# Kernel tuning notes

Hardware: AMD Instinct MI355X
Metric: run time of the kernel (lower is better)

## Reference

```python
import jax, jax.numpy as jnp
import numpy as np

B, S, D, H = 4, 2048, 512, 8
DH = D // H  # 64


def setup_inputs() -> dict:
    key = jax.random.key(0)
    ks = jax.random.split(key, 7)
    scale = 1.0 / np.sqrt(D)
    return {
        "in_query": jax.random.normal(ks[0], (B, S, D), dtype=jnp.float32),
        "in_key": jax.random.normal(ks[1], (B, S, D), dtype=jnp.float32),
        "in_value": jax.random.normal(ks[2], (B, S, D), dtype=jnp.float32),
        "W_q": jax.random.normal(ks[3], (D, D), dtype=jnp.float32) * scale,
        "W_k": jax.random.normal(ks[4], (D, D), dtype=jnp.float32) * scale,
        "W_v": jax.random.normal(ks[5], (D, D), dtype=jnp.float32) * scale,
        "W_out": jax.random.normal(ks[6], (D, D), dtype=jnp.float32) * scale,
    }


def _split_heads(x):
    # [B, S, D] -> [B, H, S, DH]
    return x.reshape(B, S, H, DH).transpose(0, 2, 1, 3)


def reference(in_query, in_key, in_value, W_q, W_k, W_v, W_out):
    q = _split_heads(in_query @ W_q)   # [B,H,S,DH]
    k = _split_heads(in_key @ W_k)
    v = _split_heads(in_value @ W_v)
    scores = jnp.einsum("bhqd,bhkd->bhqk", q, k) / jnp.sqrt(jnp.float32(DH))
    attn = jax.nn.softmax(scores, axis=-1)  # dropout p=0 -> identity
    out = jnp.einsum("bhqk,bhkd->bhqd", attn, v)  # [B,H,S,DH]
    out = out.transpose(0, 2, 1, 3).reshape(B, S, D)
    return out @ W_out
```

## Files before the change

kernel.cpp:

```cpp
#include <hip/hip_runtime.h>
#include <hip/hip_bf16.h>
#include <cstdint>
#include <cstddef>


typedef __bf16 bf16;
typedef __attribute__((ext_vector_type(8))) __bf16 bf16x8;
typedef __attribute__((ext_vector_type(4))) __bf16 bf16x4;
typedef __attribute__((ext_vector_type(4))) float floatx4;

#define MFMA16(a, b, c) __builtin_amdgcn_mfma_f32_16x16x32_bf16(a, b, c, 0, 0, 0)

#define GLD16(gp, lp)                                              \
  __builtin_amdgcn_global_load_lds(                                \
      (const __attribute__((address_space(1))) unsigned int*)(gp), \
      (__attribute__((address_space(3))) unsigned int*)(lp), 16, 0, 0)

#define PIPE_TOP()                                     \
  do {                                                 \
    asm volatile("s_waitcnt vmcnt(0)" ::: "memory");   \
    __builtin_amdgcn_s_barrier();                      \
    __builtin_amdgcn_sched_barrier(0);                 \
  } while (0)

__device__ __forceinline__ void split2(float x, bf16& hi, bf16& lo) {
  hi = (bf16)x;
  lo = (bf16)(x - (float)hi);
}

__global__ __launch_bounds__(256) void k_split_w(
    const float* __restrict__ Wq, const float* __restrict__ Wk,
    const float* __restrict__ Wv, const float* __restrict__ Wo,
    bf16* __restrict__ wt_hi, bf16* __restrict__ wt_lo) {
  __shared__ float tile[64][65];
  const int w = blockIdx.z;
  const float* W = (w == 0) ? Wq : (w == 1) ? Wk : (w == 2) ? Wv : Wo;
  const int kb = blockIdx.y * 64, nb = blockIdx.x * 64;
  const int tid = threadIdx.x;
  const int col = tid & 63, rbase = tid >> 6;
#pragma unroll
  for (int i = 0; i < 16; i++) {
    int row = rbase + i * 4;
    tile[row][col] = W[(size_t)(kb + row) * 512 + nb + col];
  }
  __syncthreads();
#pragma unroll
  for (int i = 0; i < 16; i++) {
    int nrow = rbase + i * 4;
    float v = tile[col][nrow];
    bf16 hi, lo;
    split2(v, hi, lo);
    size_t o = (size_t)w * 262144 + (size_t)(nb + nrow) * 512 + (kb + col);
    wt_hi[o] = hi;
    wt_lo[o] = lo;
  }
}

__global__ __launch_bounds__(256, 2) void k_proj_qkv(
    const float* __restrict__ Xq, const float* __restrict__ Xk,
    const float* __restrict__ Xv,
    const bf16* __restrict__ wt_hi, const bf16* __restrict__ wt_lo,
    bf16* __restrict__ Q_hi, bf16* __restrict__ Q_lo,
    bf16* __restrict__ K, bf16* __restrict__ Vt) {
  const int P = blockIdx.x;
  const int c_all = P >> 5, within = P & 31;
  const int n_idx = within >> 3, i8 = within & 7;
  const int which = c_all >> 3;
  const int g = ((c_all & 7) << 3) | i8;
  const int m0 = g * 128, n0 = n_idx * 128;

  const float* X = (which == 0) ? Xq : (which == 1) ? Xk : Xv;
  const uint8_t* Bhb = (const uint8_t*)(wt_hi + (size_t)which * 262144);
  const uint8_t* Blb = (const uint8_t*)(wt_lo + (size_t)which * 262144);
  const uint8_t* Xb = (const uint8_t*)X;
  const int tid = threadIdx.x, wave = tid >> 6, lane = tid & 63;
  const int l15 = lane & 15, l4 = lane >> 4;
  const int Am0 = (wave & 1) * 64, Bn0 = (wave >> 1) * 64;

  __shared__ float sA[2][128 * 32];
  __shared__ bf16 sBh[2][128 * 32], sBl[2][128 * 32];

  int aoff[4], adst[4];
#pragma unroll
  for (int p = 0; p < 4; p++) {
    int slot = p * 256 + tid;
    int row = slot >> 3, phys = slot & 7, lg = phys ^ (row & 7);
    aoff[p] = (m0 + row) * 2048 + lg * 16;
    adst[p] = slot * 16;
  }
  int boff[2], bdst[2];
#pragma unroll
  for (int p = 0; p < 2; p++) {
    int slot = p * 256 + tid;
    int row = slot >> 2, phys = slot & 3, lg = phys ^ (row & 3);
    boff[p] = (n0 + row) * 1024 + lg * 16;
    bdst[p] = slot * 16;
  }

  floatx4 acc[4][4];
#pragma unroll
  for (int i = 0; i < 4; i++)
#pragma unroll
    for (int j = 0; j < 4; j++) acc[i][j] = {0.f, 0.f, 0.f, 0.f};

#pragma unroll
  for (int p = 0; p < 4; p++) GLD16(Xb + aoff[p], (char*)sA[0] + adst[p]);
#pragma unroll
  for (int p = 0; p < 2; p++) {
    GLD16(Bhb + boff[p], (char*)sBh[0] + bdst[p]);
    GLD16(Blb + boff[p], (char*)sBl[0] + bdst[p]);
  }

  int cur = 0;
  for (int kb = 0; kb < 512; kb += 32) {
    PIPE_TOP();

    const char* cA = (const char*)sA[cur];
    const char* cBh = (const char*)sBh[cur];
    const char* cBl = (const char*)sBl[cur];

    floatx4 af0[4], af1[4];
    bf16x8 bhf[4], blf[4];
#pragma unroll
    for (int mt = 0; mt < 4; mt++) {
      int row = Am0 + mt * 16 + l15, r7 = row & 7;
      af0[mt] = *(const floatx4*)(cA + row * 128 + (((2 * l4) ^ r7) * 16));
      af1[mt] = *(const floatx4*)(cA + row * 128 + (((2 * l4 + 1) ^ r7) * 16));
    }
#pragma unroll
    for (int nt = 0; nt < 4; nt++) {
      int row = Bn0 + nt * 16 + l15, r3 = row & 3;
      bhf[nt] = *(const bf16x8*)(cBh + row * 64 + ((l4 ^ r3) * 16));
      blf[nt] = *(const bf16x8*)(cBl + row * 64 + ((l4 ^ r3) * 16));
    }

    if (kb + 32 < 512) {
      const int nx = cur ^ 1, nkb = kb + 32;
#pragma unroll
      for (int p = 0; p < 4; p++)
        GLD16(Xb + aoff[p] + nkb * 4, (char*)sA[nx] + adst[p]);
#pragma unroll
      for (int p = 0; p < 2; p++) {
        GLD16(Bhb + boff[p] + nkb * 2, (char*)sBh[nx] + bdst[p]);
        GLD16(Blb + boff[p] + nkb * 2, (char*)sBl[nx] + bdst[p]);
      }
    }

    bf16x8 ah[4], al[4];
#pragma unroll
    for (int mt = 0; mt < 4; mt++) {
#pragma unroll
      for (int j = 0; j < 4; j++) {
        bf16 h, l;
        split2(af0[mt][j], h, l);
        ah[mt][j] = h; al[mt][j] = l;
        split2(af1[mt][j], h, l);
        ah[mt][4 + j] = h; al[mt][4 + j] = l;
      }
    }
#pragma unroll
    for (int nt = 0; nt < 4; nt++) {
#pragma unroll
      for (int mt = 0; mt < 4; mt++) {
        acc[mt][nt] = MFMA16(ah[mt], bhf[nt], acc[mt][nt]);
        acc[mt][nt] = MFMA16(ah[mt], blf[nt], acc[mt][nt]);
        acc[mt][nt] = MFMA16(al[mt], bhf[nt], acc[mt][nt]);
      }
    }
    cur ^= 1;
  }

  const float scale = (which == 0) ? 0.125f : (which == 1) ? 1.44269504f : 1.0f;
#pragma unroll
  for (int mt = 0; mt < 4; mt++) {
#pragma unroll
    for (int nt = 0; nt < 4; nt++) {
      int m_base = m0 + Am0 + mt * 16 + l4 * 4;
      int n = n0 + Bn0 + nt * 16 + l15;
      int h = (n >> 6) & 7, d = n & 63;
      if (which == 2) {
        int kbase = m_base & 2047, b = m_base >> 11;
        int a32 = kbase & ~31, v = (kbase >> 2) & 7;
        int sbase = a32 + 8 * (v & 3) + 4 * (v >> 2);
        bf16x4 pv;
#pragma unroll
        for (int r = 0; r < 4; r++) pv[r] = (bf16)acc[mt][nt][r];
        *(bf16x4*)&Vt[((size_t)(b * 8 + h) * 64 + d) * 2048 + sbase] = pv;
      } else {
#pragma unroll
        for (int r = 0; r < 4; r++) {
          int m = m_base + r;
          int b = m >> 11, s = m & 2047;
          float v = acc[mt][nt][r] * scale;
          size_t o = ((size_t)(b * 8 + h) * 2048 + s) * 64 + d;
          if (which == 0) {
            bf16 hi, lo;
            split2(v, hi, lo);
            Q_hi[o] = hi; Q_lo[o] = lo;
          } else {
            K[o] = (bf16)v;
          }
        }
      }
    }
  }
}

__global__ __launch_bounds__(256, 2) void k_flash(
    const bf16* __restrict__ Q_hi, const bf16* __restrict__ Q_lo,
    const bf16* __restrict__ K, const bf16* __restrict__ Vt,
    bf16* __restrict__ O_hi, bf16* __restrict__ O_lo) {
  const int P = blockIdx.x;
  const int hi4 = P >> 8, rem = P & 255;
  const int qt = rem >> 3;
  const int bh = hi4 * 8 + (rem & 7);
  const int b = bh >> 3, h = bh & 7;
  const int tid = threadIdx.x, wave = tid >> 6, lane = tid & 63;
  const int l15 = lane & 15, l4 = lane >> 4;
  const int q0 = qt * 64;

  __shared__ char smem[2 * 32768 + 1024];
  float* lbuf = (float*)(smem + 65536);

  const uint8_t* Kb = (const uint8_t*)K + (size_t)bh * 2048 * 128;
  const uint8_t* Vb = (const uint8_t*)Vt + (size_t)bh * 64 * 4096;
  int koff[4], voff[4], dst[4];
#pragma unroll
  for (int p = 0; p < 4; p++) {
    int slot = p * 256 + tid;
    {
      int row = slot >> 3, phys = slot & 7, lg = phys ^ (row & 7);
      koff[p] = row * 128 + lg * 16;
    }
    {
      int row = slot >> 4, phys = slot & 15, lg = phys ^ (row & 15);
      voff[p] = row * 4096 + lg * 16;
    }
    dst[p] = slot * 16;
  }

#pragma unroll
  for (int p = 0; p < 4; p++) {
    GLD16(Kb + koff[p], smem + dst[p]);
    GLD16(Vb + voff[p], smem + 16384 + dst[p]);
  }

  bf16x8 qh[4][2], ql[4][2];
#pragma unroll
  for (int nt = 0; nt < 4; nt++) {
    const bf16* ph = Q_hi + ((size_t)bh * 2048 + q0 + nt * 16 + l15) * 64 + l4 * 8;
    const bf16* pl = Q_lo + ((size_t)bh * 2048 + q0 + nt * 16 + l15) * 64 + l4 * 8;
    qh[nt][0] = *(const bf16x8*)ph;
    qh[nt][1] = *(const bf16x8*)(ph + 32);
    ql[nt][0] = *(const bf16x8*)pl;
    ql[nt][1] = *(const bf16x8*)(pl + 32);
  }

  float lp[4] = {0.f, 0.f, 0.f, 0.f};
  floatx4 oacc[4][4];
#pragma unroll
  for (int i = 0; i < 4; i++)
#pragma unroll
    for (int j = 0; j < 4; j++) oacc[i][j] = {0.f, 0.f, 0.f, 0.f};

  int cur = 0;
  for (int j0 = 0; j0 < 2048; j0 += 128) {
    PIPE_TOP();

    const char* sK = smem + cur * 32768;
    const char* sV = sK + 16384;

    bf16x8 kf[2][2];
#pragma unroll
    for (int kt = 0; kt < 2; kt++) {
      int row = wave * 32 + kt * 16 + l15, r7 = row & 7;
#pragma unroll
      for (int ks = 0; ks < 2; ks++)
        kf[ks][kt] =
            *(const bf16x8*)(sK + row * 128 + (((ks * 4 + l4) ^ r7) * 16));
    }
    bf16x8 vf[4];
#pragma unroll
    for (int nt = 0; nt < 4; nt++) {
      int row = nt * 16 + l15;
      vf[nt] =
          *(const bf16x8*)(sV + row * 256 + (((wave * 4 + l4) ^ l15) * 16));
    }

    if (j0 + 128 < 2048) {
      char* nb = smem + (cur ^ 1) * 32768;
      const size_t nj = (size_t)(j0 + 128);
#pragma unroll
      for (int p = 0; p < 4; p++) {
        GLD16(Kb + nj * 128 + koff[p], nb + dst[p]);
        GLD16(Vb + nj * 2 + voff[p], nb + 16384 + dst[p]);
      }
    }

    floatx4 sc[2][4];
#pragma unroll
    for (int kt = 0; kt < 2; kt++)
#pragma unroll
      for (int nt = 0; nt < 4; nt++)
        sc[kt][nt] = {-24.f, -24.f, -24.f, -24.f};
#pragma unroll
    for (int ks = 0; ks < 2; ks++) {
#pragma unroll
      for (int nt = 0; nt < 4; nt++) {
        sc[0][nt] = MFMA16(kf[ks][0], qh[nt][ks], sc[0][nt]);
        sc[0][nt] = MFMA16(kf[ks][0], ql[nt][ks], sc[0][nt]);
        sc[1][nt] = MFMA16(kf[ks][1], qh[nt][ks], sc[1][nt]);
        sc[1][nt] = MFMA16(kf[ks][1], ql[nt][ks], sc[1][nt]);
      }
    }

    bf16x8 pf[4];
#pragma unroll
    for (int nt = 0; nt < 4; nt++) {
#pragma unroll
      for (int r = 0; r < 4; r++) {
        float p0 = __builtin_amdgcn_exp2f(sc[0][nt][r]);
        float p1 = __builtin_amdgcn_exp2f(sc[1][nt][r]);
        lp[nt] += p0 + p1;
        pf[nt][r] = (bf16)p0;
        pf[nt][4 + r] = (bf16)p1;
      }
    }

#pragma unroll
    for (int nt = 0; nt < 4; nt++) {
#pragma unroll
      for (int mq = 0; mq < 4; mq++)
        oacc[mq][nt] = MFMA16(pf[mq], vf[nt], oacc[mq][nt]);
    }
    cur ^= 1;
  }

#pragma unroll
  for (int nt = 0; nt < 4; nt++) {
    lp[nt] += __shfl_xor(lp[nt], 16, 64);
    lp[nt] += __shfl_xor(lp[nt], 32, 64);
  }
  __syncthreads();
  if (l4 == 0) {
#pragma unroll
    for (int nt = 0; nt < 4; nt++) lbuf[wave * 64 + nt * 16 + l15] = lp[nt];
  }
  floatx4* red = (floatx4*)smem;
#pragma unroll
  for (int phase = 0; phase < 2; phase++) {
    if (wave >= 1) {
#pragma unroll
      for (int i = 0; i < 8; i++) {
        int mq = phase * 2 + (i >> 2);
        red[(wave - 1) * 512 + i * 64 + lane] = oacc[mq][i & 3];
      }
    }
    __syncthreads();
    if (wave == 0) {
#pragma unroll
      for (int i = 0; i < 8; i++) {
        int mq = phase * 2 + (i >> 2);
        oacc[mq][i & 3] += red[i * 64 + lane] + red[512 + i * 64 + lane] +
                           red[1024 + i * 64 + lane];
      }
    }
    __syncthreads();
  }
  if (wave == 0) {
    float lt[4];
#pragma unroll
    for (int nt = 0; nt < 4; nt++)
      lt[nt] = lbuf[nt * 16 + l15] + lbuf[64 + nt * 16 + l15] +
               lbuf[128 + nt * 16 + l15] + lbuf[192 + nt * 16 + l15];
    float rl[4][4];
#pragma unroll
    for (int mq = 0; mq < 4; mq++)
#pragma unroll
      for (int r = 0; r < 4; r++)
        rl[mq][r] = 1.0f / __shfl(lt[mq], (lane & 48) | (l4 * 4 + r), 64);
#pragma unroll
    for (int mq = 0; mq < 4; mq++) {
#pragma unroll
      for (int nt = 0; nt < 4; nt++) {
#pragma unroll
        for (int r = 0; r < 4; r++) {
          float v = oacc[mq][nt][r] * rl[mq][r];
          int gs = q0 + mq * 16 + l4 * 4 + r;
          int gd = h * 64 + nt * 16 + l15;
          size_t o = ((size_t)b * 2048 + gs) * 512 + gd;
          bf16 hi, lo;
          split2(v, hi, lo);
          O_hi[o] = hi;
          O_lo[o] = lo;
        }
      }
    }
  }
}

__global__ __launch_bounds__(256, 2) void k_proj_out(
    const bf16* __restrict__ O_hi, const bf16* __restrict__ O_lo,
    const bf16* __restrict__ wt_hi, const bf16* __restrict__ wt_lo,
    float* __restrict__ out) {
  const int P = blockIdx.x;
  const int c = P >> 5, within = P & 31;
  const int n_idx = within >> 3, i8 = within & 7;
  const int g = (c << 3) | i8;
  const int m0 = g * 128, n0 = n_idx * 128;

  const uint8_t* Ahb = (const uint8_t*)O_hi;
  const uint8_t* Alb = (const uint8_t*)O_lo;
  const uint8_t* Bhb = (const uint8_t*)(wt_hi + (size_t)3 * 262144);
  const uint8_t* Blb = (const uint8_t*)(wt_lo + (size_t)3 * 262144);
  const int tid = threadIdx.x, wave = tid >> 6, lane = tid & 63;
  const int l15 = lane & 15, l4 = lane >> 4;
  const int Am0 = (wave & 1) * 64, Bn0 = (wave >> 1) * 64;

  __shared__ bf16 sAh[2][128 * 32], sAl[2][128 * 32];
  __shared__ bf16 sBh[2][128 * 32], sBl[2][128 * 32];

  int aoff[2], boff[2], dst[2];
#pragma unroll
  for (int p = 0; p < 2; p++) {
    int slot = p * 256 + tid;
    int row = slot >> 2, phys = slot & 3, lg = phys ^ (row & 3);
    aoff[p] = (m0 + row) * 1024 + lg * 16;
    boff[p] = (n0 + row) * 1024 + lg * 16;
    dst[p] = slot * 16;
  }

  floatx4 acc[4][4];
#pragma unroll
  for (int i = 0; i < 4; i++)
#pragma unroll
    for (int j = 0; j < 4; j++) acc[i][j] = {0.f, 0.f, 0.f, 0.f};

#pragma unroll
  for (int p = 0; p < 2; p++) {
    GLD16(Ahb + aoff[p], (char*)sAh[0] + dst[p]);
    GLD16(Alb + aoff[p], (char*)sAl[0] + dst[p]);
    GLD16(Bhb + boff[p], (char*)sBh[0] + dst[p]);
    GLD16(Blb + boff[p], (char*)sBl[0] + dst[p]);
  }

  int cur = 0;
  for (int kb = 0; kb < 512; kb += 32) {
    PIPE_TOP();

    const char* cAh = (const char*)sAh[cur];
    const char* cAl = (const char*)sAl[cur];
    const char* cBh = (const char*)sBh[cur];
    const char* cBl = (const char*)sBl[cur];

    bf16x8 ah[4], al[4], bhf[4], blf[4];
#pragma unroll
    for (int mt = 0; mt < 4; mt++) {
      int row = Am0 + mt * 16 + l15, r3 = row & 3;
      ah[mt] = *(const bf16x8*)(cAh + row * 64 + ((l4 ^ r3) * 16));
      al[mt] = *(const bf16x8*)(cAl + row * 64 + ((l4 ^ r3) * 16));
    }
#pragma unroll
    for (int nt = 0; nt < 4; nt++) {
      int row = Bn0 + nt * 16 + l15, r3 = row & 3;
      bhf[nt] = *(const bf16x8*)(cBh + row * 64 + ((l4 ^ r3) * 16));
      blf[nt] = *(const bf16x8*)(cBl + row * 64 + ((l4 ^ r3) * 16));
    }

    if (kb + 32 < 512) {
      const int nx = cur ^ 1, nkb = kb + 32;
#pragma unroll
      for (int p = 0; p < 2; p++) {
        GLD16(Ahb + aoff[p] + nkb * 2, (char*)sAh[nx] + dst[p]);
        GLD16(Alb + aoff[p] + nkb * 2, (char*)sAl[nx] + dst[p]);
        GLD16(Bhb + boff[p] + nkb * 2, (char*)sBh[nx] + dst[p]);
        GLD16(Blb + boff[p] + nkb * 2, (char*)sBl[nx] + dst[p]);
      }
    }

#pragma unroll
    for (int nt = 0; nt < 4; nt++) {
#pragma unroll
      for (int mt = 0; mt < 4; mt++) {
        acc[mt][nt] = MFMA16(ah[mt], bhf[nt], acc[mt][nt]);
        acc[mt][nt] = MFMA16(ah[mt], blf[nt], acc[mt][nt]);
        acc[mt][nt] = MFMA16(al[mt], bhf[nt], acc[mt][nt]);
      }
    }
    cur ^= 1;
  }
#pragma unroll
  for (int mt = 0; mt < 4; mt++) {
#pragma unroll
    for (int nt = 0; nt < 4; nt++) {
#pragma unroll
      for (int r = 0; r < 4; r++) {
        int m = m0 + Am0 + mt * 16 + l4 * 4 + r;
        int n = n0 + Bn0 + nt * 16 + l15;
        out[(size_t)m * 512 + n] = acc[mt][nt][r];
      }
    }
  }
}

extern "C" void kernel_launch(void* const* d_in, const int* in_sizes, int n_in,
                              void* d_out, int out_size, void* d_ws, size_t ws_size,
                              hipStream_t stream) {
  (void)in_sizes; (void)n_in; (void)out_size; (void)ws_size;
  const float* Xq = (const float*)d_in[0];
  const float* Xk = (const float*)d_in[1];
  const float* Xv = (const float*)d_in[2];
  const float* Wq = (const float*)d_in[3];
  const float* Wk = (const float*)d_in[4];
  const float* Wv = (const float*)d_in[5];
  const float* Wo = (const float*)d_in[6];
  float* out = (float*)d_out;

  char* ws = (char*)d_ws;
  size_t off = 0;
  auto alloc = [&](size_t n) {
    void* p = ws + off;
    off += (n + 255) & ~(size_t)255;
    return p;
  };
  const size_t NW = 4 * 262144;
  const size_t NE = 4194304;
  bf16* wt_hi = (bf16*)alloc(NW * 2);
  bf16* wt_lo = (bf16*)alloc(NW * 2);
  bf16* Qh = (bf16*)alloc(NE * 2);
  bf16* Ql = (bf16*)alloc(NE * 2);
  bf16* Kk = (bf16*)alloc(NE * 2);
  bf16* Vt = (bf16*)alloc(NE * 2);
  bf16* Oh = (bf16*)alloc(NE * 2);
  bf16* Ol = (bf16*)alloc(NE * 2);

  k_split_w<<<dim3(8, 8, 4), dim3(256), 0, stream>>>(Wq, Wk, Wv, Wo, wt_hi, wt_lo);
  k_proj_qkv<<<dim3(768), dim3(256), 0, stream>>>(Xq, Xk, Xv, wt_hi, wt_lo,
                                                  Qh, Ql, Kk, Vt);
  k_flash<<<dim3(1024), dim3(256), 0, stream>>>(Qh, Ql, Kk, Vt, Oh, Ol);
  k_proj_out<<<dim3(256), dim3(256), 0, stream>>>(Oh, Ol, wt_hi, wt_lo, out);
}
```

Before: 222.2 us.

## Load A operand and V fragments directly from global into registers

In the QKV projection, the fp32 activation tile is no longer staged through LDS. Each lane loads its A fragments straight from global memory into registers, prefetched one k-step ahead. In the flash kernel, V fragments are read directly from global memory each iteration instead of being double-buffered in LDS. Both changes cut shared-memory use so launch bounds can be raised to 3 blocks per CU for more occupancy. The trade-off is uncoalesced, non-prefetched global loads (especially V in flash, loaded after the barrier with no overlap) and more register pressure under the tighter launch bound.

```diff
diff --git a/kernel.cpp b/kernel.cpp
--- a/kernel.cpp
+++ b/kernel.cpp
@@ -56,7 +56,7 @@
   }
 }
 
-__global__ __launch_bounds__(256, 2) void k_proj_qkv(
+__global__ __launch_bounds__(256, 3) void k_proj_qkv(
     const float* __restrict__ Xq, const float* __restrict__ Xk,
     const float* __restrict__ Xv,
     const bf16* __restrict__ wt_hi, const bf16* __restrict__ wt_lo,
@@ -77,16 +77,13 @@
   const int l15 = lane & 15, l4 = lane >> 4;
   const int Am0 = (wave & 1) * 64, Bn0 = (wave >> 1) * 64;
 
-  __shared__ float sA[2][128 * 32];
   __shared__ bf16 sBh[2][128 * 32], sBl[2][128 * 32];
 
-  int aoff[4], adst[4];
-#pragma unroll
-  for (int p = 0; p < 4; p++) {
-    int slot = p * 256 + tid;
-    int row = slot >> 3, phys = slot & 7, lg = phys ^ (row & 7);
-    aoff[p] = (m0 + row) * 2048 + lg * 16;
-    adst[p] = slot * 16;
+  const uint8_t* aptr[4];
+#pragma unroll
+  for (int mt = 0; mt < 4; mt++) {
+    int row = m0 + Am0 + mt * 16 + l15;
+    aptr[mt] = Xb + (size_t)row * 2048 + l4 * 32;
   }
   int boff[2], bdst[2];
 #pragma unroll
@@ -104,29 +101,26 @@
     for (int j = 0; j < 4; j++) acc[i][j] = {0.f, 0.f, 0.f, 0.f};
 
 #pragma unroll
-  for (int p = 0; p < 4; p++) GLD16(Xb + aoff[p], (char*)sA[0] + adst[p]);
-#pragma unroll
   for (int p = 0; p < 2; p++) {
     GLD16(Bhb + boff[p], (char*)sBh[0] + bdst[p]);
     GLD16(Blb + boff[p], (char*)sBl[0] + bdst[p]);
   }
+  floatx4 af0c[4], af1c[4];
+#pragma unroll
+  for (int mt = 0; mt < 4; mt++) {
+    af0c[mt] = *(const floatx4*)(aptr[mt]);
+    af1c[mt] = *(const floatx4*)(aptr[mt] + 16);
+  }
 
   int cur = 0;
+#pragma unroll 2
   for (int kb = 0; kb < 512; kb += 32) {
     PIPE_TOP();
 
-    const char* cA = (const char*)sA[cur];
     const char* cBh = (const char*)sBh[cur];
     const char* cBl = (const char*)sBl[cur];
 
-    floatx4 af0[4], af1[4];
     bf16x8 bhf[4], blf[4];
-#pragma unroll
-    for (int mt = 0; mt < 4; mt++) {
-      int row = Am0 + mt * 16 + l15, r7 = row & 7;
-      af0[mt] = *(const floatx4*)(cA + row * 128 + (((2 * l4) ^ r7) * 16));
-      af1[mt] = *(const floatx4*)(cA + row * 128 + (((2 * l4 + 1) ^ r7) * 16));
-    }
 #pragma unroll
     for (int nt = 0; nt < 4; nt++) {
       int row = Bn0 + nt * 16 + l15, r3 = row & 3;
@@ -134,16 +128,19 @@
       blf[nt] = *(const bf16x8*)(cBl + row * 64 + ((l4 ^ r3) * 16));
     }
 
+    floatx4 af0n[4], af1n[4];
     if (kb + 32 < 512) {
       const int nx = cur ^ 1, nkb = kb + 32;
-#pragma unroll
-      for (int p = 0; p < 4; p++)
-        GLD16(Xb + aoff[p] + nkb * 4, (char*)sA[nx] + adst[p]);
 #pragma unroll
       for (int p = 0; p < 2; p++) {
         GLD16(Bhb + boff[p] + nkb * 2, (char*)sBh[nx] + bdst[p]);
         GLD16(Blb + boff[p] + nkb * 2, (char*)sBl[nx] + bdst[p]);
       }
+#pragma unroll
+      for (int mt = 0; mt < 4; mt++) {
+        af0n[mt] = *(const floatx4*)(aptr[mt] + nkb * 4);
+        af1n[mt] = *(const floatx4*)(aptr[mt] + nkb * 4 + 16);
+      }
     }
 
     bf16x8 ah[4], al[4];
@@ -152,9 +149,9 @@
 #pragma unroll
       for (int j = 0; j < 4; j++) {
         bf16 h, l;
-        split2(af0[mt][j], h, l);
+        split2(af0c[mt][j], h, l);
         ah[mt][j] = h; al[mt][j] = l;
-        split2(af1[mt][j], h, l);
+        split2(af1c[mt][j], h, l);
         ah[mt][4 + j] = h; al[mt][4 + j] = l;
       }
     }
@@ -166,6 +163,11 @@
         acc[mt][nt] = MFMA16(ah[mt], blf[nt], acc[mt][nt]);
         acc[mt][nt] = MFMA16(al[mt], bhf[nt], acc[mt][nt]);
       }
+    }
+#pragma unroll
+    for (int mt = 0; mt < 4; mt++) {
+      af0c[mt] = af0n[mt];
+      af1c[mt] = af1n[mt];
     }
     cur ^= 1;
   }
@@ -206,7 +208,7 @@
   }
 }
 
-__global__ __launch_bounds__(256, 2) void k_flash(
+__global__ __launch_bounds__(256, 3) void k_flash(
     const bf16* __restrict__ Q_hi, const bf16* __restrict__ Q_lo,
     const bf16* __restrict__ K, const bf16* __restrict__ Vt,
     bf16* __restrict__ O_hi, bf16* __restrict__ O_lo) {
@@ -219,31 +221,22 @@
   const int l15 = lane & 15, l4 = lane >> 4;
   const int q0 = qt * 64;
 
-  __shared__ char smem[2 * 32768 + 1024];
-  float* lbuf = (float*)(smem + 65536);
+  __shared__ char smem[2 * 16384 + 1024];
+  float* lbuf = (float*)(smem + 32768);
 
   const uint8_t* Kb = (const uint8_t*)K + (size_t)bh * 2048 * 128;
   const uint8_t* Vb = (const uint8_t*)Vt + (size_t)bh * 64 * 4096;
-  int koff[4], voff[4], dst[4];
+  int koff[4], dst[4];
 #pragma unroll
   for (int p = 0; p < 4; p++) {
     int slot = p * 256 + tid;
-    {
-      int row = slot >> 3, phys = slot & 7, lg = phys ^ (row & 7);
-      koff[p] = row * 128 + lg * 16;
-    }
-    {
-      int row = slot >> 4, phys = slot & 15, lg = phys ^ (row & 15);
-      voff[p] = row * 4096 + lg * 16;
-    }
+    int row = slot >> 3, phys = slot & 7, lg = phys ^ (row & 7);
+    koff[p] = row * 128 + lg * 16;
     dst[p] = slot * 16;
   }
 
 #pragma unroll
-  for (int p = 0; p < 4; p++) {
-    GLD16(Kb + koff[p], smem + dst[p]);
-    GLD16(Vb + voff[p], smem + 16384 + dst[p]);
-  }
+  for (int p = 0; p < 4; p++) GLD16(Kb + koff[p], smem + dst[p]);
 
   bf16x8 qh[4][2], ql[4][2];
 #pragma unroll
@@ -267,9 +260,15 @@
   for (int j0 = 0; j0 < 2048; j0 += 128) {
     PIPE_TOP();
 
-    const char* sK = smem + cur * 32768;
-    const char* sV = sK + 16384;
-
+    bf16x8 vf[4];
+#pragma unroll
+    for (int nt = 0; nt < 4; nt++) {
+      int row = nt * 16 + l15;
+      vf[nt] = *(const bf16x8*)(Vb + (size_t)row * 4096 + j0 * 2 +
+                                (wave * 4 + l4) * 16);
+    }
+
+    const char* sK = smem + cur * 16384;
     bf16x8 kf[2][2];
 #pragma unroll
     for (int kt = 0; kt < 2; kt++) {
@@ -279,22 +278,12 @@
         kf[ks][kt] =
             *(const bf16x8*)(sK + row * 128 + (((ks * 4 + l4) ^ r7) * 16));
     }
-    bf16x8 vf[4];
-#pragma unroll
-    for (int nt = 0; nt < 4; nt++) {
-      int row = nt * 16 + l15;
-      vf[nt] =
-          *(const bf16x8*)(sV + row * 256 + (((wave * 4 + l4) ^ l15) * 16));
-    }
 
     if (j0 + 128 < 2048) {
-      char* nb = smem + (cur ^ 1) * 32768;
+      char* nb = smem + (cur ^ 1) * 16384;
       const size_t nj = (size_t)(j0 + 128);
 #pragma unroll
-      for (int p = 0; p < 4; p++) {
-        GLD16(Kb + nj * 128 + koff[p], nb + dst[p]);
-        GLD16(Vb + nj * 2 + voff[p], nb + 16384 + dst[p]);
-      }
+      for (int p = 0; p < 4; p++) GLD16(Kb + nj * 128 + koff[p], nb + dst[p]);
     }
 
     floatx4 sc[2][4];
```

New measurement: 403.6 us. +81.6%, slower.

## Single-buffer LDS in all GEMM/flash kernels and raise occupancy to three blocks

Applied to the files above, without the earlier changes.

Replaces double-buffered LDS staging with a single buffer in the QKV projection, flash attention and output projection kernels. A new LDS-wait-plus-barrier is placed before the next prefetch so the buffer can be overwritten safely. Occupancy hints are raised from two to three blocks per CU. Flash now keeps Q hi/lo fragments in LDS instead of registers, and the output projection uses 64-row tiles with twice as many blocks. The aim is more resident waves and better CU fill, at the cost of an extra barrier per iteration and less overlap between loads and compute.

```diff
diff --git a/kernel.cpp b/kernel.cpp
--- a/kernel.cpp
+++ b/kernel.cpp
@@ -19,6 +19,14 @@
 #define PIPE_TOP()                                     \
   do {                                                 \
     asm volatile("s_waitcnt vmcnt(0)" ::: "memory");   \
+    __builtin_amdgcn_s_barrier();                      \
+    __builtin_amdgcn_sched_barrier(0);                 \
+  } while (0)
+
+#define LGKM_BARRIER()                                 \
+  do {                                                 \
+    asm volatile("s_waitcnt lgkmcnt(0)" ::: "memory"); \
+    __builtin_amdgcn_sched_barrier(0);                 \
     __builtin_amdgcn_s_barrier();                      \
     __builtin_amdgcn_sched_barrier(0);                 \
   } while (0)
@@ -56,7 +64,7 @@
   }
 }
 
-__global__ __launch_bounds__(256, 2) void k_proj_qkv(
+__global__ __launch_bounds__(256, 3) void k_proj_qkv(
     const float* __restrict__ Xq, const float* __restrict__ Xk,
     const float* __restrict__ Xv,
     const bf16* __restrict__ wt_hi, const bf16* __restrict__ wt_lo,
@@ -77,8 +85,8 @@
   const int l15 = lane & 15, l4 = lane >> 4;
   const int Am0 = (wave & 1) * 64, Bn0 = (wave >> 1) * 64;
 
-  __shared__ float sA[2][128 * 32];
-  __shared__ bf16 sBh[2][128 * 32], sBl[2][128 * 32];
+  __shared__ float sA[128 * 32];
+  __shared__ bf16 sBh[128 * 32], sBl[128 * 32];
 
   int aoff[4], adst[4];
 #pragma unroll
@@ -104,45 +112,42 @@
     for (int j = 0; j < 4; j++) acc[i][j] = {0.f, 0.f, 0.f, 0.f};
 
 #pragma unroll
-  for (int p = 0; p < 4; p++) GLD16(Xb + aoff[p], (char*)sA[0] + adst[p]);
+  for (int p = 0; p < 4; p++) GLD16(Xb + aoff[p], (char*)sA + adst[p]);
 #pragma unroll
   for (int p = 0; p < 2; p++) {
-    GLD16(Bhb + boff[p], (char*)sBh[0] + bdst[p]);
-    GLD16(Blb + boff[p], (char*)sBl[0] + bdst[p]);
-  }
-
-  int cur = 0;
+    GLD16(Bhb + boff[p], (char*)sBh + bdst[p]);
+    GLD16(Blb + boff[p], (char*)sBl + bdst[p]);
+  }
+
   for (int kb = 0; kb < 512; kb += 32) {
     PIPE_TOP();
 
-    const char* cA = (const char*)sA[cur];
-    const char* cBh = (const char*)sBh[cur];
-    const char* cBl = (const char*)sBl[cur];
-
     floatx4 af0[4], af1[4];
     bf16x8 bhf[4], blf[4];
 #pragma unroll
     for (int mt = 0; mt < 4; mt++) {
       int row = Am0 + mt * 16 + l15, r7 = row & 7;
-      af0[mt] = *(const floatx4*)(cA + row * 128 + (((2 * l4) ^ r7) * 16));
-      af1[mt] = *(const floatx4*)(cA + row * 128 + (((2 * l4 + 1) ^ r7) * 16));
+      af0[mt] = *(const floatx4*)((const char*)sA + row * 128 + (((2 * l4) ^ r7) * 16));
+      af1[mt] = *(const floatx4*)((const char*)sA + row * 128 + (((2 * l4 + 1) ^ r7) * 16));
     }
 #pragma unroll
     for (int nt = 0; nt < 4; nt++) {
       int row = Bn0 + nt * 16 + l15, r3 = row & 3;
-      bhf[nt] = *(const bf16x8*)(cBh + row * 64 + ((l4 ^ r3) * 16));
-      blf[nt] = *(const bf16x8*)(cBl + row * 64 + ((l4 ^ r3) * 16));
-    }
+      bhf[nt] = *(const bf16x8*)((const char*)sBh + row * 64 + ((l4 ^ r3) * 16));
+      blf[nt] = *(const bf16x8*)((const char*)sBl + row * 64 + ((l4 ^ r3) * 16));
+    }
+
+    LGKM_BARRIER();
 
     if (kb + 32 < 512) {
-      const int nx = cur ^ 1, nkb = kb + 32;
+      const int nkb = kb + 32;
 #pragma unroll
       for (int p = 0; p < 4; p++)
-        GLD16(Xb + aoff[p] + nkb * 4, (char*)sA[nx] + adst[p]);
+        GLD16(Xb + aoff[p] + nkb * 4, (char*)sA + adst[p]);
 #pragma unroll
       for (int p = 0; p < 2; p++) {
-        GLD16(Bhb + boff[p] + nkb * 2, (char*)sBh[nx] + bdst[p]);
-        GLD16(Blb + boff[p] + nkb * 2, (char*)sBl[nx] + bdst[p]);
+        GLD16(Bhb + boff[p] + nkb * 2, (char*)sBh + bdst[p]);
+        GLD16(Blb + boff[p] + nkb * 2, (char*)sBl + bdst[p]);
       }
     }
 
@@ -167,7 +172,6 @@
         acc[mt][nt] = MFMA16(al[mt], bhf[nt], acc[mt][nt]);
       }
     }
-    cur ^= 1;
   }
 
   const float scale = (which == 0) ? 0.125f : (which == 1) ? 1.44269504f : 1.0f;
@@ -206,7 +210,7 @@
   }
 }
 
-__global__ __launch_bounds__(256, 2) void k_flash(
+__global__ __launch_bounds__(256, 3) void k_flash(
     const bf16* __restrict__ Q_hi, const bf16* __restrict__ Q_lo,
     const bf16* __restrict__ K, const bf16* __restrict__ Vt,
     bf16* __restrict__ O_hi, bf16* __restrict__ O_lo) {
@@ -219,8 +223,8 @@
   const int l15 = lane & 15, l4 = lane >> 4;
   const int q0 = qt * 64;
 
-  __shared__ char smem[2 * 32768 + 1024];
-  float* lbuf = (float*)(smem + 65536);
+  __shared__ char smem[50176];
+  float* lbuf = (float*)(smem + 49152);
 
   const uint8_t* Kb = (const uint8_t*)K + (size_t)bh * 2048 * 128;
   const uint8_t* Vb = (const uint8_t*)Vt + (size_t)bh * 64 * 4096;
@@ -245,15 +249,19 @@
     GLD16(Vb + voff[p], smem + 16384 + dst[p]);
   }
 
-  bf16x8 qh[4][2], ql[4][2];
 #pragma unroll
   for (int nt = 0; nt < 4; nt++) {
-    const bf16* ph = Q_hi + ((size_t)bh * 2048 + q0 + nt * 16 + l15) * 64 + l4 * 8;
-    const bf16* pl = Q_lo + ((size_t)bh * 2048 + q0 + nt * 16 + l15) * 64 + l4 * 8;
-    qh[nt][0] = *(const bf16x8*)ph;
-    qh[nt][1] = *(const bf16x8*)(ph + 32);
-    ql[nt][0] = *(const bf16x8*)pl;
-    ql[nt][1] = *(const bf16x8*)(pl + 32);
+#pragma unroll
+    for (int ks = 0; ks < 2; ks++) {
+      const bf16* ph =
+          Q_hi + ((size_t)bh * 2048 + q0 + nt * 16 + l15) * 64 + ks * 32 + l4 * 8;
+      const bf16* pl =
+          Q_lo + ((size_t)bh * 2048 + q0 + nt * 16 + l15) * 64 + ks * 32 + l4 * 8;
+      *(bf16x8*)(smem + 32768 + ((nt * 2 + ks) * 64 + lane) * 16) =
+          *(const bf16x8*)ph;
+      *(bf16x8*)(smem + 40960 + ((nt * 2 + ks) * 64 + lane) * 16) =
+          *(const bf16x8*)pl;
+    }
   }
 
   float lp[4] = {0.f, 0.f, 0.f, 0.f};
@@ -263,12 +271,13 @@
 #pragma unroll
     for (int j = 0; j < 4; j++) oacc[i][j] = {0.f, 0.f, 0.f, 0.f};
 
-  int cur = 0;
+  __syncthreads();
+
   for (int j0 = 0; j0 < 2048; j0 += 128) {
     PIPE_TOP();
 
-    const char* sK = smem + cur * 32768;
-    const char* sV = sK + 16384;
+    const char* sK = smem;
+    const char* sV = smem + 16384;
 
     bf16x8 kf[2][2];
 #pragma unroll
@@ -287,13 +296,14 @@
           *(const bf16x8*)(sV + row * 256 + (((wave * 4 + l4) ^ l15) * 16));
     }
 
+    LGKM_BARRIER();
+
     if (j0 + 128 < 2048) {
-      char* nb = smem + (cur ^ 1) * 32768;
       const size_t nj = (size_t)(j0 + 128);
 #pragma unroll
       for (int p = 0; p < 4; p++) {
-        GLD16(Kb + nj * 128 + koff[p], nb + dst[p]);
-        GLD16(Vb + nj * 2 + voff[p], nb + 16384 + dst[p]);
+        GLD16(Kb + nj * 128 + koff[p], smem + dst[p]);
+        GLD16(Vb + nj * 2 + voff[p], smem + 16384 + dst[p]);
       }
     }
 
@@ -307,10 +317,14 @@
     for (int ks = 0; ks < 2; ks++) {
 #pragma unroll
       for (int nt = 0; nt < 4; nt++) {
-        sc[0][nt] = MFMA16(kf[ks][0], qh[nt][ks], sc[0][nt]);
-        sc[0][nt] = MFMA16(kf[ks][0], ql[nt][ks], sc[0][nt]);
-        sc[1][nt] = MFMA16(kf[ks][1], qh[nt][ks], sc[1][nt]);
-        sc[1][nt] = MFMA16(kf[ks][1], ql[nt][ks], sc[1][nt]);
+        bf16x8 qhf =
+            *(const bf16x8*)(smem + 32768 + ((nt * 2 + ks) * 64 + lane) * 16);
+        bf16x8 qlf =
+            *(const bf16x8*)(smem + 40960 + ((nt * 2 + ks) * 64 + lane) * 16);
+        sc[0][nt] = MFMA16(kf[ks][0], qhf, sc[0][nt]);
+        sc[0][nt] = MFMA16(kf[ks][0], qlf, sc[0][nt]);
+        sc[1][nt] = MFMA16(kf[ks][1], qhf, sc[1][nt]);
+        sc[1][nt] = MFMA16(kf[ks][1], qlf, sc[1][nt]);
       }
     }
 
@@ -333,7 +347,6 @@
       for (int mq = 0; mq < 4; mq++)
         oacc[mq][nt] = MFMA16(pf[mq], vf[nt], oacc[mq][nt]);
     }
-    cur ^= 1;
   }
 
 #pragma unroll
@@ -404,10 +417,8 @@
     const bf16* __restrict__ wt_hi, const bf16* __restrict__ wt_lo,
     float* __restrict__ out) {
   const int P = blockIdx.x;
-  const int c = P >> 5, within = P & 31;
-  const int n_idx = within >> 3, i8 = within & 7;
-  const int g = (c << 3) | i8;
-  const int m0 = g * 128, n0 = n_idx * 128;
+  const int g = P & 127, n_idx = P >> 7;
+  const int m0 = g * 64, n0 = n_idx * 128;
 
   const uint8_t* Ahb = (const uint8_t*)O_hi;
   const uint8_t* Alb = (const uint8_t*)O_lo;
@@ -415,82 +426,83 @@
   const uint8_t* Blb = (const uint8_t*)(wt_lo + (size_t)3 * 262144);
   const int tid = threadIdx.x, wave = tid >> 6, lane = tid & 63;
   const int l15 = lane & 15, l4 = lane >> 4;
-  const int Am0 = (wave & 1) * 64, Bn0 = (wave >> 1) * 64;
-
-  __shared__ bf16 sAh[2][128 * 32], sAl[2][128 * 32];
-  __shared__ bf16 sBh[2][128 * 32], sBl[2][128 * 32];
-
-  int aoff[2], boff[2], dst[2];
+  const int Am0 = (wave & 1) * 32, Bn0 = (wave >> 1) * 64;
+
+  __shared__ bf16 sAh[64 * 32], sAl[64 * 32];
+  __shared__ bf16 sBh[128 * 32], sBl[128 * 32];
+
+  int aoff, adst;
+  {
+    int slot = tid;
+    int row = slot >> 2, phys = slot & 3, lg = phys ^ (row & 3);
+    aoff = (m0 + row) * 1024 + lg * 16;
+    adst = slot * 16;
+  }
+  int boff[2], bdst[2];
 #pragma unroll
   for (int p = 0; p < 2; p++) {
     int slot = p * 256 + tid;
     int row = slot >> 2, phys = slot & 3, lg = phys ^ (row & 3);
-    aoff[p] = (m0 + row) * 1024 + lg * 16;
     boff[p] = (n0 + row) * 1024 + lg * 16;
-    dst[p] = slot * 16;
-  }
-
-  floatx4 acc[4][4];
-#pragma unroll
-  for (int i = 0; i < 4; i++)
+    bdst[p] = slot * 16;
+  }
+
+  floatx4 acc[2][4];
+#pragma unroll
+  for (int i = 0; i < 2; i++)
 #pragma unroll
     for (int j = 0; j < 4; j++) acc[i][j] = {0.f, 0.f, 0.f, 0.f};
 
+  GLD16(Ahb + aoff, (char*)sAh + adst);
+  GLD16(Alb + aoff, (char*)sAl + adst);
 #pragma unroll
   for (int p = 0; p < 2; p++) {
-    GLD16(Ahb + aoff[p], (char*)sAh[0] + dst[p]);
-    GLD16(Alb + aoff[p], (char*)sAl[0] + dst[p]);
-    GLD16(Bhb + boff[p], (char*)sBh[0] + dst[p]);
-    GLD16(Blb + boff[p], (char*)sBl[0] + dst[p]);
-  }
-
-  int cur = 0;
+    GLD16(Bhb + boff[p], (char*)sBh + bdst[p]);
+    GLD16(Blb + boff[p], (char*)sBl + bdst[p]);
+  }
+
   for (int kb = 0; kb < 512; kb += 32) {
     PIPE_TOP();
 
-    const char* cAh = (const char*)sAh[cur];
-    const char* cAl = (const char*)sAl[cur];
-    const char* cBh = (const char*)sBh[cur];
-    const char* cBl = (const char*)sBl[cur];
-
-    bf16x8 ah[4], al[4], bhf[4], blf[4];
-#pragma unroll
-    for (int mt = 0; mt < 4; mt++) {
+    bf16x8 ah[2], al[2], bhf[4], blf[4];
+#pragma unroll
+    for (int mt = 0; mt < 2; mt++) {
       int row = Am0 + mt * 16 + l15, r3 = row & 3;
-      ah[mt] = *(const bf16x8*)(cAh + row * 64 + ((l4 ^ r3) * 16));
-      al[mt] = *(const bf16x8*)(cAl + row * 64 + ((l4 ^ r3) * 16));
+      ah[mt] = *(const bf16x8*)((const char*)sAh + row * 64 + ((l4 ^ r3) * 16));
+      al[mt] = *(const bf16x8*)((const char*)sAl + row * 64 + ((l4 ^ r3) * 16));
     }
 #pragma unroll
     for (int nt = 0; nt < 4; nt++) {
       int row = Bn0 + nt * 16 + l15, r3 = row & 3;
-      bhf[nt] = *(const bf16x8*)(cBh + row * 64 + ((l4 ^ r3) * 16));
-      blf[nt] = *(const bf16x8*)(cBl + row * 64 + ((l4 ^ r3) * 16));
-    }
+      bhf[nt] = *(const bf16x8*)((const char*)sBh + row * 64 + ((l4 ^ r3) * 16));
+      blf[nt] = *(const bf16x8*)((const char*)sBl + row * 64 + ((l4 ^ r3) * 16));
+    }
+
+    LGKM_BARRIER();
 
     if (kb + 32 < 512) {
-      const int nx = cur ^ 1, nkb = kb + 32;
+      const int nkb = kb + 32;
+      GLD16(Ahb + aoff + nkb * 2, (char*)sAh + adst);
+      GLD16(Alb + aoff + nkb * 2, (char*)sAl + adst);
 #pragma unroll
       for (int p = 0; p < 2; p++) {
-        GLD16(Ahb + aoff[p] + nkb * 2, (char*)sAh[nx] + dst[p]);
-        GLD16(Alb + aoff[p] + nkb * 2, (char*)sAl[nx] + dst[p]);
-        GLD16(Bhb + boff[p] + nkb * 2, (char*)sBh[nx] + dst[p]);
-        GLD16(Blb + boff[p] + nkb * 2, (char*)sBl[nx] + dst[p]);
-      }
-    }
-
-#pragma unroll
-    for (int nt = 0; nt < 4; nt++) {
-#pragma unroll
-      for (int mt = 0; mt < 4; mt++) {
+        GLD16(Bhb + boff[p] + nkb * 2, (char*)sBh + bdst[p]);
+        GLD16(Blb + boff[p] + nkb * 2, (char*)sBl + bdst[p]);
+      }
+    }
+
+#pragma unroll
+    for (int nt = 0; nt < 4; nt++) {
+#pragma unroll
+      for (int mt = 0; mt < 2; mt++) {
         acc[mt][nt] = MFMA16(ah[mt], bhf[nt], acc[mt][nt]);
         acc[mt][nt] = MFMA16(ah[mt], blf[nt], acc[mt][nt]);
         acc[mt][nt] = MFMA16(al[mt], bhf[nt], acc[mt][nt]);
       }
     }
-    cur ^= 1;
-  }
-#pragma unroll
-  for (int mt = 0; mt < 4; mt++) {
+  }
+#pragma unroll
+  for (int mt = 0; mt < 2; mt++) {
 #pragma unroll
     for (int nt = 0; nt < 4; nt++) {
 #pragma unroll
@@ -538,5 +550,5 @@
   k_proj_qkv<<<dim3(768), dim3(256), 0, stream>>>(Xq, Xk, Xv, wt_hi, wt_lo,
                                                   Qh, Ql, Kk, Vt);
   k_flash<<<dim3(1024), dim3(256), 0, stream>>>(Qh, Ql, Kk, Vt, Oh, Ol);
-  k_proj_out<<<dim3(256), dim3(256), 0, stream>>>(Oh, Ol, wt_hi, wt_lo, out);
+  k_proj_out<<<dim3(512), dim3(256), 0, stream>>>(Oh, Ol, wt_hi, wt_lo, out);
 }
```

Result: no change. 218.6 us (-1.6%).
